# Kernel tuning notes

Hardware: AMD Instinct MI355X
Metric: run time of the kernel (lower is better)

The kernel has to match this reference:

```python
import jax, jax.numpy as jnp
import numpy as np
import math

B, N, IN_DIM = 128, 100, 8
E, H, FF, L = 512, 8, 2048, 6
DH = E // H
MAX_STEPS = int(N * 1.5)
EPS = 1e-5

def _ln(x, g, b):
    mu = x.mean(-1, keepdims=True)
    var = ((x - mu) ** 2).mean(-1, keepdims=True)
    return (x - mu) / jnp.sqrt(var + EPS) * g + b

def _mha(q_in, k_in, v_in, wq, bq, wk, bk, wv, bv, wo, bo):
    Bq, Sq = q_in.shape[0], q_in.shape[1]
    q = (q_in @ wq + bq).reshape(Bq, Sq, H, DH)
    k = (k_in @ wk + bk).reshape(Bq, -1, H, DH)
    v = (v_in @ wv + bv).reshape(Bq, -1, H, DH)
    s = jnp.einsum('bqhd,bkhd->bhqk', q, k) / math.sqrt(DH)
    a = jax.nn.softmax(s, axis=-1)
    o = jnp.einsum('bhqk,bkhd->bqhd', a, v).reshape(Bq, Sq, E)
    return o @ wo + bo

def setup_inputs():
    key = jax.random.key(0)
    keys = iter(jax.random.split(key, 64))
    def nrm(shape, s=0.02):
        return jax.random.normal(next(keys), shape, jnp.float32) * s
    d = {}
    d['node_features'] = jax.random.normal(next(keys), (B, N, IN_DIM), jnp.float32)
    d['edge_weights'] = jax.random.uniform(next(keys), (B, N, N), jnp.float32)
    pos = np.arange(N)[:, None].astype(np.float32)
    div = np.exp(np.arange(0, E, 2).astype(np.float32) * (-math.log(10000.0) / E))
    pe = np.zeros((N, E), np.float32)
    pe[:, 0::2] = np.sin(pos * div); pe[:, 1::2] = np.cos(pos * div)
    d['pe'] = jnp.asarray(pe)
    d['in_w'] = nrm((IN_DIM, E)); d['in_b'] = jnp.zeros((E,), jnp.float32)
    for nm in ['enc_wq', 'enc_wk', 'enc_wv', 'enc_wo']:
        d[nm] = nrm((L, E, E))
    for nm in ['enc_bq', 'enc_bk', 'enc_bv', 'enc_bo']:
        d[nm] = jnp.zeros((L, E), jnp.float32)
    d['enc_w1'] = nrm((L, E, FF)); d['enc_b1'] = jnp.zeros((L, FF), jnp.float32)
    d['enc_w2'] = nrm((L, FF, E)); d['enc_b2'] = jnp.zeros((L, E), jnp.float32)
    d['enc_ln1g'] = jnp.ones((L, E), jnp.float32); d['enc_ln1b'] = jnp.zeros((L, E), jnp.float32)
    d['enc_ln2g'] = jnp.ones((L, E), jnp.float32); d['enc_ln2b'] = jnp.zeros((L, E), jnp.float32)
    d['lstm_wih'] = nrm((E, 4 * E)); d['lstm_whh'] = nrm((E, 4 * E))
    d['lstm_bih'] = jnp.zeros((4 * E,), jnp.float32); d['lstm_bhh'] = jnp.zeros((4 * E,), jnp.float32)
    for nm in ['dec_wq', 'dec_wk', 'dec_wv', 'dec_wo', 'dec_pw']:
        d[nm] = nrm((E, E))
    for nm in ['dec_bq', 'dec_bk', 'dec_bv', 'dec_bo', 'dec_pb']:
        d[nm] = jnp.zeros((E,), jnp.float32)
    d['dec_lng'] = jnp.ones((E,), jnp.float32); d['dec_lnb'] = jnp.zeros((E,), jnp.float32)
    d['shortcut_bonus'] = jnp.asarray(5.0, jnp.float32)
    d['revisit_penalty'] = jnp.asarray(-0.5, jnp.float32)
    d['done_w'] = nrm((E, 1)); d['done_b'] = jnp.zeros((1,), jnp.float32)
    return d

def _forward(node_features, edge_weights, pe, in_w, in_b, enc_wq, enc_bq, enc_wk, enc_bk, enc_wv, enc_bv, enc_wo, enc_bo, enc_w1, enc_b1, enc_w2, enc_b2, enc_ln1g, enc_ln1b, enc_ln2g, enc_ln2b, lstm_wih, lstm_whh, lstm_bih, lstm_bhh, dec_wq, dec_bq, dec_wk, dec_bk, dec_wv, dec_bv, dec_wo, dec_bo, dec_pw, dec_pb, dec_lng, dec_lnb, shortcut_bonus, revisit_penalty, done_w, done_b):
    # ---- Encoder (dropout = eval-mode identity) ----
    x = node_features @ in_w + in_b + pe[:N]
    for l in range(L):
        attn = _mha(x, x, x, enc_wq[l], enc_bq[l], enc_wk[l], enc_bk[l], enc_wv[l], enc_bv[l], enc_wo[l], enc_bo[l])
        x = _ln(x + attn, enc_ln1g[l], enc_ln1b[l])
        ff = jax.nn.relu(x @ enc_w1[l] + enc_b1[l]) @ enc_w2[l] + enc_b2[l]
        x = _ln(x + ff, enc_ln2g[l], enc_ln2b[l])
    node_emb = x  # [B, N, E]

    ar = jnp.arange(N)
    ew_to_first = edge_weights[:, :, 0]  # dist(mid -> node 0), [B, N]

    def step_fn(carry, step):
        h, c, ctx, visited, ucount, complete, all_vis, first, prev = carry
        # LSTMCell, torch gate order (i, f, g, o)
        gates = ctx @ lstm_wih + lstm_bih + h @ lstm_whh + lstm_bhh
        i_g, f_g, g_g, o_g = jnp.split(gates, 4, axis=-1)
        c2 = jax.nn.sigmoid(f_g) * c + jax.nn.sigmoid(i_g) * jnp.tanh(g_g)
        h2 = jax.nn.sigmoid(o_g) * jnp.tanh(c2)
        # greedy done-predictor: stop if sigmoid(logit) > 0.5 once tour can be closed
        done_p = jax.nn.sigmoid(h2 @ done_w + done_b)[:, 0]
        eligible = (~complete) & (ucount >= N) & (step >= N)
        complete = complete | (eligible & (done_p > 0.5))
        # DecoderStep: 1-query attention over node embeddings
        a = _mha(h2[:, None, :], node_emb, node_emb, dec_wq, dec_bq, dec_wk, dec_bk, dec_wv, dec_bv, dec_wo, dec_bo)[:, 0]
        a = _ln(a, dec_lng, dec_lnb)
        logits = a @ dec_pw + dec_pb
        scores = jnp.einsum('be,bne->bn', logits, node_emb)
        # revisit penalty while tour incomplete (vectorized masked_fill_)
        scores = jnp.where((~all_vis)[:, None] & visited, revisit_penalty, scores)
        # shortcut bonus once all nodes visited (vectorized gather over edge_weights)
        ew_prev = jnp.take_along_axis(edge_weights, prev[:, None, None], axis=1)[:, 0, :]  # [B, N] row dist(prev -> *)
        direct = ew_prev[:, :1]                      # dist(prev -> 0)
        via = ew_prev + ew_to_first                  # dist(prev -> mid) + dist(mid -> 0)
        bonus = jnp.where(via < direct, shortcut_bonus * (direct - via) / direct, 0.0)
        scores = scores + jnp.where(all_vis[:, None], bonus, 0.0)
        # completed tours: force return to first node
        scores = jnp.where(complete[:, None], -1e9, scores)
        scores = jnp.where(complete[:, None] & (ar[None, :] == first[:, None]), 100.0, scores)
        probs = jax.nn.softmax(scores, axis=1)
        curr = jnp.argmax(probs, axis=1).astype(jnp.int32)  # greedy selection
        logp = jnp.log(jnp.take_along_axis(probs, curr[:, None], 1)[:, 0] + 1e-10)
        first = jnp.where(step == 0, curr, first)
        # state updates (guarded by active, as in the torch per-batch loop)
        active = ~complete
        cur_mask = ar[None, :] == curr[:, None]
        newly = active & ~jnp.take_along_axis(visited, curr[:, None], 1)[:, 0]
        ucount = ucount + newly.astype(jnp.int32)
        visited = visited | (active[:, None] & cur_mask)
        all_vis = all_vis | (ucount >= N)
        ctx2 = jnp.take_along_axis(node_emb, curr[:, None, None], axis=1)[:, 0, :]
        return (h2, c2, ctx2, visited, ucount, complete, all_vis, first, curr), (curr, logp)

    carry0 = (jnp.zeros((B, E), jnp.float32), jnp.zeros((B, E), jnp.float32), node_emb.mean(1),
              jnp.zeros((B, N), bool), jnp.zeros((B,), jnp.int32),
              jnp.zeros((B,), bool), jnp.zeros((B,), bool),
              jnp.zeros((B,), jnp.int32), jnp.zeros((B,), jnp.int32))
    carry, (tours, logps) = jax.lax.scan(step_fn, carry0, jnp.arange(MAX_STEPS))
    complete, first = carry[5], carry[7]
    # final forced step (step == max_steps in torch): incomplete tours return to first node, logp = 0
    final_node = jnp.where(complete, jnp.int32(0), first)
    tours = jnp.concatenate([tours, final_node[None]], 0)                 # [MAX_STEPS+1, B]
    logps = jnp.concatenate([logps, jnp.zeros((1, B), jnp.float32)], 0)   # [MAX_STEPS+1, B]
    return logps, tours

def reference(node_features, edge_weights, pe, in_w, in_b, enc_wq, enc_bq, enc_wk, enc_bk, enc_wv, enc_bv, enc_wo, enc_bo, enc_w1, enc_b1, enc_w2, enc_b2, enc_ln1g, enc_ln1b, enc_ln2g, enc_ln2b, lstm_wih, lstm_whh, lstm_bih, lstm_bhh, dec_wq, dec_bq, dec_wk, dec_bk, dec_wv, dec_bv, dec_wo, dec_bo, dec_pw, dec_pb, dec_lng, dec_lnb, shortcut_bonus, revisit_penalty, done_w, done_b):
    return _forward(node_features, edge_weights, pe, in_w, in_b, enc_wq, enc_bq, enc_wk, enc_bk, enc_wv, enc_bv, enc_wo, enc_bo, enc_w1, enc_b1, enc_w2, enc_b2, enc_ln1g, enc_ln1b, enc_ln2g, enc_ln2b, lstm_wih, lstm_whh, lstm_bih, lstm_bhh, dec_wq, dec_bq, dec_wk, dec_bk, dec_wv, dec_bv, dec_wo, dec_bo, dec_pw, dec_pb, dec_lng, dec_lnb, shortcut_bonus, revisit_penalty, done_w, done_b)
```

## Files before the change

### kernel.cpp

```cpp
#include <hip/hip_runtime.h>
#include <math.h>

#define Bb 128
#define Nn 100
#define Ee 512
#define Hh 8
#define DHd 64
#define FFf 2048
#define Ll 6
#define STEPS 150

typedef _Float16 h8 __attribute__((ext_vector_type(8)));
typedef _Float16 h4 __attribute__((ext_vector_type(4)));
typedef float f4 __attribute__((ext_vector_type(4)));

template<bool RELU, bool BIAS, bool OUTF32, bool SPLITK>
__global__ __launch_bounds__(256) void mgemm_k(
    const _Float16* __restrict__ Ah, const _Float16* __restrict__ Al, int lda,
    const _Float16* __restrict__ Bh, const _Float16* __restrict__ Bl, int ldb,
    float* __restrict__ C, _Float16* __restrict__ Ch, _Float16* __restrict__ Cl,
    int ldc, const float* __restrict__ bias, int K, int kc, int Mtot)
{
  __shared__ _Float16 sm[4 * 5120];
  _Float16* sAh = sm;
  _Float16* sAl = sm + 5120;
  _Float16* sBh = sm + 10240;
  _Float16* sBl = sm + 15360;
  const int tid = threadIdx.x;
  const int m0 = blockIdx.y * 128, n0 = blockIdx.x * 128;
  const int k0 = SPLITK ? blockIdx.z * kc : 0;
  const int kEnd = SPLITK ? k0 + kc : K;
  const int lane = tid & 63, wave = tid >> 6;
  const int wm = wave >> 1, wn = wave & 1;
  const int m16 = lane & 15, kg = lane >> 4;
  f4 acc[4][4];
#pragma unroll
  for (int i = 0; i < 4; ++i)
#pragma unroll
    for (int j = 0; j < 4; ++j) acc[i][j] = (f4)0.f;

  for (int kt = k0; kt < kEnd; kt += 32) {
#pragma unroll
    for (int it = 0; it < 2; ++it) {
      int idx = tid + it * 256;
      int row = idx >> 2, g = idx & 3;
      int lo_ = row * 40 + g * 8;
      size_t ga = (size_t)(m0 + row) * lda + kt + g * 8;
      size_t gb = (size_t)(n0 + row) * ldb + kt + g * 8;
      *(h8*)(sAh + lo_) = *(const h8*)(Ah + ga);
      *(h8*)(sAl + lo_) = *(const h8*)(Al + ga);
      *(h8*)(sBh + lo_) = *(const h8*)(Bh + gb);
      *(h8*)(sBl + lo_) = *(const h8*)(Bl + gb);
    }
    __syncthreads();
    h8 a_h[4], a_l[4], b_h[4], b_l[4];
#pragma unroll
    for (int i = 0; i < 4; ++i) {
      int ro = (wm * 64 + i * 16 + m16) * 40 + kg * 8;
      int co = (wn * 64 + i * 16 + m16) * 40 + kg * 8;
      a_h[i] = *(const h8*)(sAh + ro);
      a_l[i] = *(const h8*)(sAl + ro);
      b_h[i] = *(const h8*)(sBh + co);
      b_l[i] = *(const h8*)(sBl + co);
    }
#pragma unroll
    for (int i = 0; i < 4; ++i)
#pragma unroll
      for (int j = 0; j < 4; ++j) {
        acc[i][j] = __builtin_amdgcn_mfma_f32_16x16x32_f16(a_h[i], b_h[j], acc[i][j], 0, 0, 0);
        acc[i][j] = __builtin_amdgcn_mfma_f32_16x16x32_f16(a_h[i], b_l[j], acc[i][j], 0, 0, 0);
        acc[i][j] = __builtin_amdgcn_mfma_f32_16x16x32_f16(a_l[i], b_h[j], acc[i][j], 0, 0, 0);
      }
    __syncthreads();
  }

  float* Cz = OUTF32 ? (C + (SPLITK ? (size_t)blockIdx.z * (size_t)Mtot * ldc : (size_t)0)) : C;
  int rb = m0 + wm * 64 + kg * 4;
  int cb = n0 + wn * 64 + m16;
#pragma unroll
  for (int j = 0; j < 4; ++j) {
    int col = cb + j * 16;
    float bv = BIAS ? bias[col] : 0.f;
#pragma unroll
    for (int i = 0; i < 4; ++i) {
#pragma unroll
      for (int r = 0; r < 4; ++r) {
        float v = acc[i][j][r] + bv;
        if (RELU) v = fmaxf(v, 0.f);
        int row = rb + i * 16 + r;
        if (OUTF32) {
          Cz[(size_t)row * ldc + col] = v;
        } else {
          _Float16 hh = (_Float16)v;
          Ch[(size_t)row * ldc + col] = hh;
          Cl[(size_t)row * ldc + col] = (_Float16)(v - (float)hh);
        }
      }
    }
  }
}

__global__ __launch_bounds__(256) void wconv_k(
    const float* __restrict__ W, int K, int N,
    _Float16* __restrict__ Th, _Float16* __restrict__ Tl)
{
  __shared__ float t[32][33];
  int n0 = blockIdx.x * 32, k0 = blockIdx.y * 32;
  int tid = threadIdx.x;
  int r = tid >> 3, c4 = (tid & 7) * 4;
  float4 v = *(const float4*)(W + (size_t)(k0 + r) * N + n0 + c4);
  t[r][c4 + 0] = v.x; t[r][c4 + 1] = v.y; t[r][c4 + 2] = v.z; t[r][c4 + 3] = v.w;
  __syncthreads();
  h4 hi, lo;
#pragma unroll
// ... 76 lines not shown
  const float* qg = q + ((size_t)b * Nn) * 512 + h * 64;
  const float* kg = k + ((size_t)b * Nn) * 512 + h * 64;
  const float* vg = v + ((size_t)b * Nn) * 512 + h * 64;
  for (int idx = t; idx < 6400; idx += 256) {
    int i = idx >> 6, d = idx & 63;
    qs[i * 68 + d]  = qg[(size_t)i * 512 + d];
    kT[d * 113 + i] = kg[(size_t)i * 512 + d];
  }
  __syncthreads();
  int ti = t >> 4, tj = t & 15;
  int i0 = ti * 7, j0 = tj * 7;
  float s[7][7];
#pragma unroll
  for (int r = 0; r < 7; ++r)
#pragma unroll
    for (int c = 0; c < 7; ++c) s[r][c] = 0.f;
  for (int kk = 0; kk < 64; ++kk) {
    float a[7], bb[7];
#pragma unroll
    for (int r = 0; r < 7; ++r) a[r] = qs[(i0 + r) * 68 + kk];
#pragma unroll
    for (int c = 0; c < 7; ++c) bb[c] = kT[kk * 113 + j0 + c];
#pragma unroll
    for (int r = 0; r < 7; ++r)
#pragma unroll
      for (int c = 0; c < 7; ++c) s[r][c] += a[r] * bb[c];
  }
  __syncthreads();
#pragma unroll
  for (int r = 0; r < 7; ++r)
#pragma unroll
    for (int c = 0; c < 7; ++c) {
      int i = i0 + r, j = j0 + c;
      if (i < Nn && j < Nn) p[i * 104 + j] = s[r][c] * 0.125f;
    }
  __syncthreads();
  int w = t >> 6, lane = t & 63;
  for (int i = w; i < Nn; i += 4) {
    float x0 = p[i * 104 + lane];
    float x1 = (lane < 36) ? p[i * 104 + 64 + lane] : -3.4e38f;
    float mx = fmaxf(x0, x1);
    for (int msk = 32; msk; msk >>= 1) mx = fmaxf(mx, __shfl_xor(mx, msk));
    float e0 = expf(x0 - mx);
    float e1 = (lane < 36) ? expf(x1 - mx) : 0.f;
    float ss = e0 + e1;
    for (int msk = 32; msk; msk >>= 1) ss += __shfl_xor(ss, msk);
    p[i * 104 + lane] = e0 / ss;
    if (lane < 36) p[i * 104 + 64 + lane] = e1 / ss;
  }
  __syncthreads();
  int d0 = tj * 4;
  float oa[7][4];
#pragma unroll
  for (int r = 0; r < 7; ++r)
#pragma unroll
    for (int c = 0; c < 4; ++c) oa[r][c] = 0.f;
  for (int j = 0; j < Nn; ++j) {
    float pr[7];
#pragma unroll
    for (int r = 0; r < 7; ++r) pr[r] = p[(i0 + r) * 104 + j];
    float4 vv = *(const float4*)(vg + (size_t)j * 512 + d0);
#pragma unroll
    for (int r = 0; r < 7; ++r) {
      oa[r][0] += pr[r] * vv.x; oa[r][1] += pr[r] * vv.y;
      oa[r][2] += pr[r] * vv.z; oa[r][3] += pr[r] * vv.w;
    }
  }
  size_t ob = ((size_t)b * Nn) * 512 + h * 64 + d0;
#pragma unroll
  for (int r = 0; r < 7; ++r)
    if (i0 + r < Nn) {
      h4 hv, lv;
#pragma unroll
      for (int c = 0; c < 4; ++c) {
        _Float16 hh = (_Float16)oa[r][c];
        hv[c] = hh;
        lv[c] = (_Float16)(oa[r][c] - (float)hh);
      }
      *(h4*)(oh + ob + (size_t)(i0 + r) * 512) = hv;
      *(h4*)(ol + ob + (size_t)(i0 + r) * 512) = lv;
    }
}

template<int BM, int BN, int BK, int TM, int TN>
__global__ __launch_bounds__(256) void gemm_k(
    const float* __restrict__ A, int lda,
    const float* __restrict__ B1, const float* __restrict__ B2, int splitB, int ldb,
    float* __restrict__ C, int ldc, int M, int N, int K, int kChunk)
{
  __shared__ __align__(16) float As[BK][BM + 4];
  __shared__ __align__(16) float Bs[BK][BN + 4];
  const int tid = threadIdx.x;
  const int m0 = blockIdx.y * BM;
  const int n0 = blockIdx.x * BN;
  const int k0 = blockIdx.z * kChunk;
  const int kEnd = k0 + kChunk;
  constexpr int TCOLS = BN / TN;
  const int tm = tid / TCOLS;
  const int tn = tid % TCOLS;
  float acc[TM][TN];
#pragma unroll
  for (int i = 0; i < TM; ++i)
#pragma unroll
    for (int j = 0; j < TN; ++j) acc[i][j] = 0.f;

  for (int kt = k0; kt < kEnd; kt += BK) {
    constexpr int A4 = BM * BK / 4;
    for (int c = tid; c < A4; c += 256) {
      int mm = c / (BK / 4);
      int k4 = (c % (BK / 4)) * 4;
      float4 av = *(const float4*)(A + (size_t)(m0 + mm) * lda + kt + k4);
      As[k4 + 0][mm] = av.x;
      As[k4 + 1][mm] = av.y;
      As[k4 + 2][mm] = av.z;
      As[k4 + 3][mm] = av.w;
    }
    constexpr int B4 = BK * BN / 4;
    for (int c = tid; c < B4; c += 256) {
      int kk = c / (BN / 4);
      int n4 = (c % (BN / 4)) * 4;
      int kgi = kt + kk;
      const float* Brow = (kgi < splitB) ? (B1 + (size_t)kgi * ldb)
                                         : (B2 + (size_t)(kgi - splitB) * ldb);
      *(float4*)&Bs[kk][n4] = *(const float4*)(Brow + n0 + n4);
    }
    __syncthreads();
#pragma unroll
    for (int kk = 0; kk < BK; ++kk) {
      float a[TM], b[TN];
#pragma unroll
      for (int i = 0; i < TM; ++i) a[i] = As[kk][tm * TM + i];
#pragma unroll
      for (int j = 0; j < TN; ++j) b[j] = Bs[kk][tn * TN + j];
#pragma unroll
      for (int i = 0; i < TM; ++i)
#pragma unroll
        for (int j = 0; j < TN; ++j)
          acc[i][j] += a[i] * b[j];
    }
    __syncthreads();
  }

  float* Cout = C + (size_t)blockIdx.z * (size_t)M * ldc;
#pragma unroll
  for (int i = 0; i < TM; ++i) {
    int m = m0 + tm * TM + i;
#pragma unroll
    for (int j = 0; j < TN; j += 4) {
      int n = n0 + tn * TN + j;
      float4 r;
      r.x = acc[i][j + 0]; r.y = acc[i][j + 1]; r.z = acc[i][j + 2]; r.w = acc[i][j + 3];
      *(float4*)(Cout + (size_t)m * ldc + n) = r;
    }
  }
}

__global__ __launch_bounds__(256) void init_k(
    const float* __restrict__ emb, float* __restrict__ ctxh, float* __restrict__ cbuf,
    int* visited, int* ucount, int* complete, int* allvis, int* first, int* prev,
    float* out)
{
  int b = blockIdx.x, t = threadIdx.x;
#pragma unroll
  for (int r = 0; r < 2; ++r) {
    int e = t + 256 * r;
    float s = 0.f;
    for (int i = 0; i < Nn; ++i) s += emb[((size_t)b * Nn + i) * 512 + e];
    ctxh[(size_t)b * 1024 + e] = s / 100.f;
    ctxh[(size_t)b * 1024 + 512 + e] = 0.f;
    cbuf[(size_t)b * 512 + e] = 0.f;
  }
  if (t < Nn) visited[b * Nn + t] = 0;
  if (t == 0) {
    ucount[b] = 0; complete[b] = 0; allvis[b] = 0; first[b] = 0; prev[b] = 0;
    out[150 * Bb + b] = 0.f;
  }
}

__device__ __forceinline__ float sigm(float x) { return 1.f / (1.f + expf(-x)); }

__global__ __launch_bounds__(256) void lstm_pw_k(
    const float* __restrict__ gP, const float* __restrict__ bih, const float* __restrict__ bhh,
    float* __restrict__ ctxh, float* __restrict__ cbuf,
    const float* __restrict__ done_w, const float* __restrict__ done_b,
    int* complete, const int* ucount, int step)
{
  int b = blockIdx.x, t = threadIdx.x;
  __shared__ float red[256];
  const float* g0 = gP + (size_t)b * 2048;
  const float* g1 = gP + 262144 + (size_t)b * 2048;
  float dsum = 0.f;
#pragma unroll
  for (int r = 0; r < 2; ++r) {
    int e = t + 256 * r;
    float ig = g0[e] + g1[e] + bih[e] + bhh[e];
    float fg = g0[e + 512] + g1[e + 512] + bih[e + 512] + bhh[e + 512];
    float gg = g0[e + 1024] + g1[e + 1024] + bih[e + 1024] + bhh[e + 1024];
    float og = g0[e + 1536] + g1[e + 1536] + bih[e + 1536] + bhh[e + 1536];
    float cprev = cbuf[(size_t)b * 512 + e];
    float c2 = sigm(fg) * cprev + sigm(ig) * tanhf(gg);
    float h2 = sigm(og) * tanhf(c2);
    cbuf[(size_t)b * 512 + e] = c2;
    ctxh[(size_t)b * 1024 + 512 + e] = h2;
    dsum += h2 * done_w[e];
  }
  red[t] = dsum; __syncthreads();
  for (int o = 128; o > 0; o >>= 1) { if (t < o) red[t] += red[t + o]; __syncthreads(); }
  if (t == 0) {
    float z = red[0] + done_b[0];
    if (!complete[b] && ucount[b] >= Nn && step >= Nn && z > 0.f) complete[b] = 1;
  }
}

__global__ __launch_bounds__(128) void dec_attn_k(
    const float* __restrict__ qP, const float* __restrict__ bq,
    const float* __restrict__ Kd, const float* __restrict__ Vd,
    float* __restrict__ o)
{
  int bh = blockIdx.x; int b = bh >> 3, h = bh & 7;
  int t = threadIdx.x;
  __shared__ float qh[64];
  __shared__ float p[100];
  __shared__ float red[128];
  if (t < 64) {
    float s = bq[h * 64 + t];
#pragma unroll
    for (int s8 = 0; s8 < 8; ++s8) s += qP[(size_t)s8 * 65536 + (size_t)b * 512 + h * 64 + t];
    qh[t] = s;
  }
  __syncthreads();
  float scv = -3.4e38f;
  if (t < Nn) {
    const float* kr = Kd + ((size_t)b * Nn + t) * 512 + h * 64;
    float s = 0.f;
#pragma unroll
    for (int d = 0; d < 64; ++d) s += qh[d] * kr[d];
    scv = s * 0.125f;
  }
  red[t] = scv; __syncthreads();
  for (int o2 = 64; o2 > 0; o2 >>= 1) { if (t < o2) red[t] = fmaxf(red[t], red[t + o2]); __syncthreads(); }
  float m = red[0]; __syncthreads();
  float ex = (t < Nn) ? expf(scv - m) : 0.f;
  red[t] = ex; __syncthreads();
  for (int o2 = 64; o2 > 0; o2 >>= 1) { if (t < o2) red[t] += red[t + o2]; __syncthreads(); }
  float Z = red[0];
  if (t < Nn) p[t] = ex / Z;
  __syncthreads();
  if (t < 64) {
    float acc = 0.f;
    const float* vr = Vd + (size_t)b * Nn * 512 + h * 64 + t;
    for (int j = 0; j < Nn; ++j) acc += p[j] * vr[(size_t)j * 512];
    o[(size_t)b * 512 + h * 64 + t] = acc;
  }
}

__global__ __launch_bounds__(256) void dec_ln_k(
    const float* __restrict__ woP, const float* __restrict__ bo,
    const float* __restrict__ g, const float* __restrict__ bb,
    float* __restrict__ out)
{
  int b = blockIdx.x, t = threadIdx.x;
  __shared__ float red[256];
  float v[2];
#pragma unroll
  for (int r = 0; r < 2; ++r) {
    int e = t + 256 * r;
    float s = bo[e];
#pragma unroll
    for (int s8 = 0; s8 < 8; ++s8) s += woP[(size_t)s8 * 65536 + (size_t)b * 512 + e];
    v[r] = s;
  }
  red[t] = v[0] + v[1]; __syncthreads();
  for (int o = 128; o > 0; o >>= 1) { if (t < o) red[t] += red[t + o]; __syncthreads(); }
  float mu = red[0] * (1.f / 512.f);
  __syncthreads();
  float d0 = v[0] - mu, d1 = v[1] - mu;
  red[t] = d0 * d0 + d1 * d1; __syncthreads();
  for (int o = 128; o > 0; o >>= 1) { if (t < o) red[t] += red[t + o]; __syncthreads(); }
  float inv = 1.f / sqrtf(red[0] * (1.f / 512.f) + 1e-5f);
  out[(size_t)b * 512 + t] = d0 * inv * g[t] + bb[t];
  out[(size_t)b * 512 + t + 256] = d1 * inv * g[t + 256] + bb[t + 256];
}

__global__ __launch_bounds__(256) void select_k(
    const float* __restrict__ pwP, const float* __restrict__ pb,
    const float* __restrict__ emb, const float* __restrict__ ew,
    int* visited, int* ucount, int* complete, int* allvis, int* first, int* prev,
    float* __restrict__ ctxh, float* __restrict__ out,
    const float* __restrict__ sb_p, const float* __restrict__ rp_p, int step)
{
  int b = blockIdx.x, t = threadIdx.x;
  __shared__ float logits[512];
  __shared__ float sc[128];
  __shared__ float red[256];
  __shared__ int redi[256];
#pragma unroll
  for (int r = 0; r < 2; ++r) {
    int e = t + 256 * r;
    float s = pb[e];
#pragma unroll
    for (int s8 = 0; s8 < 8; ++s8) s += pwP[(size_t)s8 * 65536 + (size_t)b * 512 + e];
    logits[e] = s;
  }
  __syncthreads();
  if (t < Nn) {
    const float* er = emb + ((size_t)b * Nn + t) * 512;
    float s = 0.f;
    for (int e = 0; e < 512; ++e) s += logits[e] * er[e];
    int av = allvis[b];
    if (!av && visited[b * Nn + t]) s = rp_p[0];
    if (av) {
      int pv = prev[b];
      float direct = ew[(size_t)b * 10000 + (size_t)pv * 100];
      float via = ew[(size_t)b * 10000 + (size_t)pv * 100 + t] + ew[(size_t)b * 10000 + (size_t)t * 100];
      if (via < direct) s += sb_p[0] * (direct - via) / direct;
    }
    if (complete[b]) s = (t == first[b]) ? 100.f : -1e9f;
    sc[t] = s;
  }
  __syncthreads();
  float vv = (t < Nn) ? sc[t] : -3.4e38f;
  int ii = (t < Nn) ? t : 0x7fffffff;
  red[t] = vv; redi[t] = ii;
  __syncthreads();
  for (int o = 128; o > 0; o >>= 1) {
    if (t < o) {
      float v2 = red[t + o]; int i2 = redi[t + o];
      if (v2 > red[t] || (v2 == red[t] && i2 < redi[t])) { red[t] = v2; redi[t] = i2; }
    }
    __syncthreads();
  }
  float m = red[0];
  int curr = redi[0];
  __syncthreads();
  float ex = (t < Nn) ? expf(sc[t] - m) : 0.f;
  red[t] = ex; __syncthreads();
  for (int o = 128; o > 0; o >>= 1) { if (t < o) red[t] += red[t + o]; __syncthreads(); }
  float Z = red[0];
  if (t == 0) {
    float pcur = expf(sc[curr] - m) / Z;
    out[step * Bb + b] = logf(pcur + 1e-10f);
    out[(151 + step) * Bb + b] = (float)curr;
    if (!complete[b]) {
      if (!visited[b * Nn + curr]) ucount[b] = ucount[b] + 1;
      visited[b * Nn + curr] = 1;
    }
    if (ucount[b] >= Nn) allvis[b] = 1;
    if (step == 0) first[b] = curr;
    prev[b] = curr;
  }
  const float* src = emb + ((size_t)b * Nn + curr) * 512;
  ctxh[(size_t)b * 1024 + t] = src[t];
  ctxh[(size_t)b * 1024 + t + 256] = src[t + 256];
}

__global__ void final_k(const int* complete, const int* first, float* out)
{
  int b = threadIdx.x;
  out[(151 + 150) * Bb + b] = complete[b] ? 0.f : (float)first[b];
}

extern "C" void kernel_launch(void* const* d_in, const int* in_sizes, int n_in,
                              void* d_out, int out_size, void* d_ws, size_t ws_size,
                              hipStream_t stream)
{
  const float* nf      = (const float*)d_in[0];
  const float* ew      = (const float*)d_in[1];
  const float* pe      = (const float*)d_in[2];
  const float* in_w    = (const float*)d_in[3];
  const float* in_b    = (const float*)d_in[4];
  const float* enc_wq  = (const float*)d_in[5];
  const float* enc_wk  = (const float*)d_in[6];
  const float* enc_wv  = (const float*)d_in[7];
  const float* enc_wo  = (const float*)d_in[8];
  const float* enc_bq  = (const float*)d_in[9];
  const float* enc_bk  = (const float*)d_in[10];
  const float* enc_bv  = (const float*)d_in[11];
  const float* enc_bo  = (const float*)d_in[12];
  const float* enc_w1  = (const float*)d_in[13];
  const float* enc_b1  = (const float*)d_in[14];
  const float* enc_w2  = (const float*)d_in[15];
  const float* enc_b2  = (const float*)d_in[16];
  const float* ln1g    = (const float*)d_in[17];
  const float* ln1b    = (const float*)d_in[18];
  const float* ln2g    = (const float*)d_in[19];
  const float* ln2b    = (const float*)d_in[20];
  const float* wih     = (const float*)d_in[21];
  const float* whh     = (const float*)d_in[22];
  const float* bih     = (const float*)d_in[23];
  const float* bhh     = (const float*)d_in[24];
  const float* dwq     = (const float*)d_in[25];
  const float* dwk     = (const float*)d_in[26];
  const float* dwv     = (const float*)d_in[27];
  const float* dwo     = (const float*)d_in[28];
  const float* dpw     = (const float*)d_in[29];
  const float* dbq     = (const float*)d_in[30];
  const float* dbk     = (const float*)d_in[31];
  const float* dbv     = (const float*)d_in[32];
  const float* dbo     = (const float*)d_in[33];
  const float* dpb     = (const float*)d_in[34];
  const float* dlng    = (const float*)d_in[35];
  const float* dlnb    = (const float*)d_in[36];
  const float* sbp     = (const float*)d_in[37];
  const float* rpp     = (const float*)d_in[38];
  const float* done_w  = (const float*)d_in[39];
  const float* done_b  = (const float*)d_in[40];
  float* out = (float*)d_out;

  const size_t SZ = 12800ull * 512;
  float* ws = (float*)d_ws;
  float* x   = ws;
  float* xq  = x + SZ;
  float* xk  = xq + SZ;
  float* xv  = xk + SZ;
  _Float16* xh = (_Float16*)(xv + SZ);
  _Float16* xl = xh + SZ;
  _Float16* oh = xl + SZ;
  _Float16* ol = oh + SZ;
  _Float16* wb = ol + SZ;
  _Float16* wqh = wb;               _Float16* wql = wqh + 262144;
  _Float16* wkh = wql + 262144;     _Float16* wkl = wkh + 262144;
  _Float16* wvh = wkl + 262144;     _Float16* wvl = wvh + 262144;
  _Float16* woh_ = wvl + 262144;    _Float16* wol_ = woh_ + 262144;
  _Float16* w1h = wol_ + 262144;    _Float16* w1l = w1h + 1048576;
  _Float16* w2h = w1l + 1048576;    _Float16* w2l = w2h + 1048576;
  float* ctxh   = (float*)(w2l + 1048576);
  float* cbuf   = ctxh + 131072;
  float* gatesP = cbuf + 65536;
  float* qP     = gatesP + 524288;
  float* woP    = qP + 524288;
  float* pwP    = woP + 524288;
  float* abuf   = pwP + 524288;
  float* dbuf   = abuf + 65536;
  int* ivis     = (int*)(dbuf + 65536);
  int* ucount   = ivis + 12800;
  int* complete = ucount + 128;
  int* allvis   = complete + 128;
  int* first    = allvis + 128;
  int* prev     = first + 128;

  input_proj_k<<<25600, 256, 0, stream>>>(nf, in_w, in_b, pe, x, xh, xl);

  for (int l = 0; l < Ll; ++l) {
    const float* wq = enc_wq + (size_t)l * 262144;
    const float* wk = enc_wk + (size_t)l * 262144;
    const float* wv = enc_wv + (size_t)l * 262144;
    const float* wo = enc_wo + (size_t)l * 262144;
    const float* bq = enc_bq + (size_t)l * 512;
    const float* bk = enc_bk + (size_t)l * 512;
    const float* bv = enc_bv + (size_t)l * 512;
    const float* bo = enc_bo + (size_t)l * 512;
    const float* w1 = enc_w1 + (size_t)l * 1048576;
    const float* b1 = enc_b1 + (size_t)l * 2048;
    const float* w2 = enc_w2 + (size_t)l * 1048576;
    const float* b2 = enc_b2 + (size_t)l * 512;

    wconv_k<<<dim3(16, 16), 256, 0, stream>>>(wq, 512, 512, wqh, wql);
    wconv_k<<<dim3(16, 16), 256, 0, stream>>>(wk, 512, 512, wkh, wkl);
    wconv_k<<<dim3(16, 16), 256, 0, stream>>>(wv, 512, 512, wvh, wvl);
    wconv_k<<<dim3(16, 16), 256, 0, stream>>>(wo, 512, 512, woh_, wol_);
    wconv_k<<<dim3(64, 16), 256, 0, stream>>>(w1, 512, 2048, w1h, w1l);
    wconv_k<<<dim3(16, 64), 256, 0, stream>>>(w2, 2048, 512, w2h, w2l);

    mgemm_k<false, true, true, false><<<dim3(4, 100), 256, 0, stream>>>(
        xh, xl, 512, wqh, wql, 512, xq, nullptr, nullptr, 512, bq, 512, 0, 0);
    mgemm_k<false, true, true, false><<<dim3(4, 100), 256, 0, stream>>>(
        xh, xl, 512, wkh, wkl, 512, xk, nullptr, nullptr, 512, bk, 512, 0, 0);
    mgemm_k<false, true, true, false><<<dim3(4, 100), 256, 0, stream>>>(
        xh, xl, 512, wvh, wvl, 512, xv, nullptr, nullptr, 512, bv, 512, 0, 0);
    enc_attn_k<<<1024, 256, 0, stream>>>(xq, xk, xv, oh, ol);
    mgemm_k<false, true, true, false><<<dim3(4, 100), 256, 0, stream>>>(
        oh, ol, 512, woh_, wol_, 512, xq, nullptr, nullptr, 512, bo, 512, 0, 0);
    ln_k<<<12800, 256, 0, stream>>>(x, xq, ln1g + l * 512, ln1b + l * 512, x, xh, xl);
    for (int c = 0; c < 4; ++c) {
      mgemm_k<true, true, false, false><<<dim3(16, 25), 256, 0, stream>>>(
          xh + (size_t)c * 3200 * 512, xl + (size_t)c * 3200 * 512, 512,
          w1h, w1l, 512, nullptr, oh, ol, 2048, b1, 512, 0, 0);
      mgemm_k<false, false, true, true><<<dim3(4, 25, 4), 256, 0, stream>>>(
          oh, ol, 2048, w2h, w2l, 2048, xv, nullptr, nullptr, 512,
          nullptr, 2048, 512, 3200);
      reduce4_k<<<6400, 256, 0, stream>>>(xv, b2, xq + (size_t)c * 3200 * 512);
    }
    ln_k<<<12800, 256, 0, stream>>>(x, xq, ln2g + l * 512, ln2b + l * 512, x, xh, xl);
  }

  wconv_k<<<dim3(16, 16), 256, 0, stream>>>(dwk, 512, 512, wqh, wql);
  wconv_k<<<dim3(16, 16), 256, 0, stream>>>(dwv, 512, 512, wkh, wkl);
  mgemm_k<false, true, true, false><<<dim3(4, 100), 256, 0, stream>>>(
      xh, xl, 512, wqh, wql, 512, xk, nullptr, nullptr, 512, dbk, 512, 0, 0);
  mgemm_k<false, true, true, false><<<dim3(4, 100), 256, 0, stream>>>(
      xh, xl, 512, wkh, wkl, 512, xv, nullptr, nullptr, 512, dbv, 512, 0, 0);
  init_k<<<128, 256, 0, stream>>>(x, ctxh, cbuf, ivis, ucount, complete, allvis, first, prev, out);

  for (int step = 0; step < STEPS; ++step) {
    gemm_k<32, 64, 16, 2, 4><<<dim3(32, 4, 2), 256, 0, stream>>>(
        ctxh, 1024, wih, whh, 512, 2048, gatesP, 2048, 128, 2048, 1024, 512);
    lstm_pw_k<<<128, 256, 0, stream>>>(gatesP, bih, bhh, ctxh, cbuf, done_w, done_b,
                                       complete, ucount, step);
    gemm_k<32, 64, 16, 2, 4><<<dim3(8, 4, 8), 256, 0, stream>>>(
        ctxh + 512, 1024, dwq, dwq, 1 << 30, 512, qP, 512, 128, 512, 512, 64);
    dec_attn_k<<<1024, 128, 0, stream>>>(qP, dbq, xk, xv, dbuf);
    gemm_k<32, 64, 16, 2, 4><<<dim3(8, 4, 8), 256, 0, stream>>>(
        dbuf, 512, dwo, dwo, 1 << 30, 512, woP, 512, 128, 512, 512, 64);
    dec_ln_k<<<128, 256, 0, stream>>>(woP, dbo, dlng, dlnb, abuf);
    gemm_k<32, 64, 16, 2, 4><<<dim3(8, 4, 8), 256, 0, stream>>>(
        abuf, 512, dpw, dpw, 1 << 30, 512, pwP, 512, 128, 512, 512, 64);
    select_k<<<128, 256, 0, stream>>>(pwP, dpb, x, ew, ivis, ucount, complete, allvis,
                                      first, prev, ctxh, out, sbp, rpp, step);
  }
  final_k<<<1, 128, 0, stream>>>(complete, first, out);
}
```

Baseline: 16.51 ms.

## Fuse decode loop into a persistent kernel with global atomic barriers

Replaces the per-step sequence of eight small decoder kernel launches with a single persistent kernel of 128 blocks that loops over all steps. Each former kernel becomes a phase separated by a device-wide barrier built from agent-scope atomics, and each block handles two GEMM tiles per phase. This targets launch and inter-kernel gap overhead on the serial decode loop. In exchange, parallelism per phase drops, every phase pays a spin-barrier cost, and correctness depends on all blocks being co-resident.

```diff
diff --git a/kernel.cpp b/kernel.cpp
--- a/kernel.cpp
+++ b/kernel.cpp
@@ -9,6 +9,7 @@
 #define FFf 2048
 #define Ll 6
 #define STEPS 150
+#define NBLK 128
 
 typedef _Float16 h8 __attribute__((ext_vector_type(8)));
 typedef _Float16 h4 __attribute__((ext_vector_type(4)));
@@ -29,7 +30,7 @@
   const int tid = threadIdx.x;
   const int m0 = blockIdx.y * 128, n0 = blockIdx.x * 128;
   const int k0 = SPLITK ? blockIdx.z * kc : 0;
-  const int kEnd = SPLITK ? k0 + kc : K;
+  const int kEnd = SPLITK ? (k0 + kc) : K;
   const int lane = tid & 63, wave = tid >> 6;
   const int wm = wave >> 1, wn = wave & 1;
   const int m16 = lane & 15, kg = lane >> 4;
@@ -272,83 +273,10 @@
     }
 }
 
-template<int BM, int BN, int BK, int TM, int TN>
-__global__ __launch_bounds__(256) void gemm_k(
-    const float* __restrict__ A, int lda,
-    const float* __restrict__ B1, const float* __restrict__ B2, int splitB, int ldb,
-    float* __restrict__ C, int ldc, int M, int N, int K, int kChunk)
-{
-  __shared__ __align__(16) float As[BK][BM + 4];
-  __shared__ __align__(16) float Bs[BK][BN + 4];
-  const int tid = threadIdx.x;
-  const int m0 = blockIdx.y * BM;
-  const int n0 = blockIdx.x * BN;
-  const int k0 = blockIdx.z * kChunk;
-  const int kEnd = k0 + kChunk;
-  constexpr int TCOLS = BN / TN;
-  const int tm = tid / TCOLS;
-  const int tn = tid % TCOLS;
-  float acc[TM][TN];
-#pragma unroll
-  for (int i = 0; i < TM; ++i)
-#pragma unroll
-    for (int j = 0; j < TN; ++j) acc[i][j] = 0.f;
-
-  for (int kt = k0; kt < kEnd; kt += BK) {
-    constexpr int A4 = BM * BK / 4;
-    for (int c = tid; c < A4; c += 256) {
-      int mm = c / (BK / 4);
-      int k4 = (c % (BK / 4)) * 4;
-      float4 av = *(const float4*)(A + (size_t)(m0 + mm) * lda + kt + k4);
-      As[k4 + 0][mm] = av.x;
-      As[k4 + 1][mm] = av.y;
-      As[k4 + 2][mm] = av.z;
-      As[k4 + 3][mm] = av.w;
-    }
-    constexpr int B4 = BK * BN / 4;
-    for (int c = tid; c < B4; c += 256) {
-      int kk = c / (BN / 4);
-      int n4 = (c % (BN / 4)) * 4;
-      int kgi = kt + kk;
-      const float* Brow = (kgi < splitB) ? (B1 + (size_t)kgi * ldb)
-                                         : (B2 + (size_t)(kgi - splitB) * ldb);
-      *(float4*)&Bs[kk][n4] = *(const float4*)(Brow + n0 + n4);
-    }
-    __syncthreads();
-#pragma unroll
-    for (int kk = 0; kk < BK; ++kk) {
-      float a[TM], b[TN];
-#pragma unroll
-      for (int i = 0; i < TM; ++i) a[i] = As[kk][tm * TM + i];
-#pragma unroll
-      for (int j = 0; j < TN; ++j) b[j] = Bs[kk][tn * TN + j];
-#pragma unroll
-      for (int i = 0; i < TM; ++i)
-#pragma unroll
-        for (int j = 0; j < TN; ++j)
-          acc[i][j] += a[i] * b[j];
-    }
-    __syncthreads();
-  }
-
-  float* Cout = C + (size_t)blockIdx.z * (size_t)M * ldc;
-#pragma unroll
-  for (int i = 0; i < TM; ++i) {
-    int m = m0 + tm * TM + i;
-#pragma unroll
-    for (int j = 0; j < TN; j += 4) {
-      int n = n0 + tn * TN + j;
-      float4 r;
-      r.x = acc[i][j + 0]; r.y = acc[i][j + 1]; r.z = acc[i][j + 2]; r.w = acc[i][j + 3];
-      *(float4*)(Cout + (size_t)m * ldc + n) = r;
-    }
-  }
-}
-
 __global__ __launch_bounds__(256) void init_k(
     const float* __restrict__ emb, float* __restrict__ ctxh, float* __restrict__ cbuf,
     int* visited, int* ucount, int* complete, int* allvis, int* first, int* prev,
-    float* out)
+    int* bars, float* out)
 {
   int b = blockIdx.x, t = threadIdx.x;
 #pragma unroll
@@ -365,189 +293,312 @@
     ucount[b] = 0; complete[b] = 0; allvis[b] = 0; first[b] = 0; prev[b] = 0;
     out[150 * Bb + b] = 0.f;
   }
+  for (int i = b * 256 + t; i < 1280; i += 128 * 256) bars[i] = 0;
 }
 
 __device__ __forceinline__ float sigm(float x) { return 1.f / (1.f + expf(-x)); }
 
-__global__ __launch_bounds__(256) void lstm_pw_k(
-    const float* __restrict__ gP, const float* __restrict__ bih, const float* __restrict__ bhh,
-    float* __restrict__ ctxh, float* __restrict__ cbuf,
-    const float* __restrict__ done_w, const float* __restrict__ done_b,
-    int* complete, const int* ucount, int step)
-{
-  int b = blockIdx.x, t = threadIdx.x;
-  __shared__ float red[256];
-  const float* g0 = gP + (size_t)b * 2048;
-  const float* g1 = gP + 262144 + (size_t)b * 2048;
-  float dsum = 0.f;
-#pragma unroll
-  for (int r = 0; r < 2; ++r) {
-    int e = t + 256 * r;
-    float ig = g0[e] + g1[e] + bih[e] + bhh[e];
-    float fg = g0[e + 512] + g1[e + 512] + bih[e + 512] + bhh[e + 512];
-    float gg = g0[e + 1024] + g1[e + 1024] + bih[e + 1024] + bhh[e + 1024];
-    float og = g0[e + 1536] + g1[e + 1536] + bih[e + 1536] + bhh[e + 1536];
-    float cprev = cbuf[(size_t)b * 512 + e];
-    float c2 = sigm(fg) * cprev + sigm(ig) * tanhf(gg);
-    float h2 = sigm(og) * tanhf(c2);
-    cbuf[(size_t)b * 512 + e] = c2;
-    ctxh[(size_t)b * 1024 + 512 + e] = h2;
-    dsum += h2 * done_w[e];
-  }
-  red[t] = dsum; __syncthreads();
-  for (int o = 128; o > 0; o >>= 1) { if (t < o) red[t] += red[t + o]; __syncthreads(); }
-  if (t == 0) {
-    float z = red[0] + done_b[0];
-    if (!complete[b] && ucount[b] >= Nn && step >= Nn && z > 0.f) complete[b] = 1;
-  }
-}
-
-__global__ __launch_bounds__(128) void dec_attn_k(
-    const float* __restrict__ qP, const float* __restrict__ bq,
-    const float* __restrict__ Kd, const float* __restrict__ Vd,
-    float* __restrict__ o)
-{
-  int bh = blockIdx.x; int b = bh >> 3, h = bh & 7;
-  int t = threadIdx.x;
-  __shared__ float qh[64];
-  __shared__ float p[100];
-  __shared__ float red[128];
-  if (t < 64) {
-    float s = bq[h * 64 + t];
-#pragma unroll
-    for (int s8 = 0; s8 < 8; ++s8) s += qP[(size_t)s8 * 65536 + (size_t)b * 512 + h * 64 + t];
-    qh[t] = s;
-  }
-  __syncthreads();
-  float scv = -3.4e38f;
-  if (t < Nn) {
-    const float* kr = Kd + ((size_t)b * Nn + t) * 512 + h * 64;
-    float s = 0.f;
-#pragma unroll
-    for (int d = 0; d < 64; ++d) s += qh[d] * kr[d];
-    scv = s * 0.125f;
-  }
-  red[t] = scv; __syncthreads();
-  for (int o2 = 64; o2 > 0; o2 >>= 1) { if (t < o2) red[t] = fmaxf(red[t], red[t + o2]); __syncthreads(); }
-  float m = red[0]; __syncthreads();
-  float ex = (t < Nn) ? expf(scv - m) : 0.f;
-  red[t] = ex; __syncthreads();
-  for (int o2 = 64; o2 > 0; o2 >>= 1) { if (t < o2) red[t] += red[t + o2]; __syncthreads(); }
-  float Z = red[0];
-  if (t < Nn) p[t] = ex / Z;
-  __syncthreads();
-  if (t < 64) {
-    float acc = 0.f;
-    const float* vr = Vd + (size_t)b * Nn * 512 + h * 64 + t;
-    for (int j = 0; j < Nn; ++j) acc += p[j] * vr[(size_t)j * 512];
-    o[(size_t)b * 512 + h * 64 + t] = acc;
-  }
-}
-
-__global__ __launch_bounds__(256) void dec_ln_k(
-    const float* __restrict__ woP, const float* __restrict__ bo,
-    const float* __restrict__ g, const float* __restrict__ bb,
-    float* __restrict__ out)
-{
-  int b = blockIdx.x, t = threadIdx.x;
-  __shared__ float red[256];
-  float v[2];
-#pragma unroll
-  for (int r = 0; r < 2; ++r) {
-    int e = t + 256 * r;
-    float s = bo[e];
-#pragma unroll
-    for (int s8 = 0; s8 < 8; ++s8) s += woP[(size_t)s8 * 65536 + (size_t)b * 512 + e];
-    v[r] = s;
-  }
-  red[t] = v[0] + v[1]; __syncthreads();
-  for (int o = 128; o > 0; o >>= 1) { if (t < o) red[t] += red[t + o]; __syncthreads(); }
-  float mu = red[0] * (1.f / 512.f);
-  __syncthreads();
-  float d0 = v[0] - mu, d1 = v[1] - mu;
-  red[t] = d0 * d0 + d1 * d1; __syncthreads();
-  for (int o = 128; o > 0; o >>= 1) { if (t < o) red[t] += red[t + o]; __syncthreads(); }
-  float inv = 1.f / sqrtf(red[0] * (1.f / 512.f) + 1e-5f);
-  out[(size_t)b * 512 + t] = d0 * inv * g[t] + bb[t];
-  out[(size_t)b * 512 + t + 256] = d1 * inv * g[t + 256] + bb[t + 256];
-}
-
-__global__ __launch_bounds__(256) void select_k(
-    const float* __restrict__ pwP, const float* __restrict__ pb,
-    const float* __restrict__ emb, const float* __restrict__ ew,
-    int* visited, int* ucount, int* complete, int* allvis, int* first, int* prev,
-    float* __restrict__ ctxh, float* __restrict__ out,
-    const float* __restrict__ sb_p, const float* __restrict__ rp_p, int step)
-{
-  int b = blockIdx.x, t = threadIdx.x;
-  __shared__ float logits[512];
-  __shared__ float sc[128];
-  __shared__ float red[256];
-  __shared__ int redi[256];
-#pragma unroll
-  for (int r = 0; r < 2; ++r) {
-    int e = t + 256 * r;
-    float s = pb[e];
-#pragma unroll
-    for (int s8 = 0; s8 < 8; ++s8) s += pwP[(size_t)s8 * 65536 + (size_t)b * 512 + e];
-    logits[e] = s;
-  }
-  __syncthreads();
-  if (t < Nn) {
-    const float* er = emb + ((size_t)b * Nn + t) * 512;
-    float s = 0.f;
-    for (int e = 0; e < 512; ++e) s += logits[e] * er[e];
-    int av = allvis[b];
-    if (!av && visited[b * Nn + t]) s = rp_p[0];
-    if (av) {
-      int pv = prev[b];
-      float direct = ew[(size_t)b * 10000 + (size_t)pv * 100];
-      float via = ew[(size_t)b * 10000 + (size_t)pv * 100 + t] + ew[(size_t)b * 10000 + (size_t)t * 100];
-      if (via < direct) s += sb_p[0] * (direct - via) / direct;
-    }
-    if (complete[b]) s = (t == first[b]) ? 100.f : -1e9f;
-    sc[t] = s;
-  }
-  __syncthreads();
-  float vv = (t < Nn) ? sc[t] : -3.4e38f;
-  int ii = (t < Nn) ? t : 0x7fffffff;
-  red[t] = vv; redi[t] = ii;
-  __syncthreads();
-  for (int o = 128; o > 0; o >>= 1) {
-    if (t < o) {
-      float v2 = red[t + o]; int i2 = redi[t + o];
-      if (v2 > red[t] || (v2 == red[t] && i2 < redi[t])) { red[t] = v2; redi[t] = i2; }
+__device__ __forceinline__ void gbar(int* bars, int slot)
+{
+  __syncthreads();
+  if (threadIdx.x == 0) {
+    __threadfence();
+    __hip_atomic_fetch_add(&bars[slot], 1, __ATOMIC_RELEASE, __HIP_MEMORY_SCOPE_AGENT);
+    while (__hip_atomic_load(&bars[slot], __ATOMIC_ACQUIRE, __HIP_MEMORY_SCOPE_AGENT) < NBLK)
+      __builtin_amdgcn_s_sleep(1);
+    __threadfence();
+  }
+  __syncthreads();
+}
+
+__device__ void gemm_dev(
+    int bx, int by, int bz,
+    const float* __restrict__ A, int lda,
+    const float* __restrict__ B1, const float* __restrict__ B2, int splitB, int ldb,
+    float* __restrict__ C, int ldc, int kChunk, char* smraw)
+{
+  float (*As)[36] = (float(*)[36])smraw;
+  float (*Bs)[68] = (float(*)[68])(smraw + 2304);
+  const int tid = threadIdx.x;
+  const int m0 = by * 32, n0 = bx * 64;
+  const int k0 = bz * kChunk, kEnd = k0 + kChunk;
+  const int tm = tid >> 4, tn = tid & 15;
+  float acc[2][4];
+#pragma unroll
+  for (int i = 0; i < 2; ++i)
+#pragma unroll
+    for (int j = 0; j < 4; ++j) acc[i][j] = 0.f;
+
+  for (int kt = k0; kt < kEnd; kt += 16) {
+    for (int c = tid; c < 128; c += 256) {
+      int mm = c >> 2;
+      int k4 = (c & 3) * 4;
+      float4 av = *(const float4*)(A + (size_t)(m0 + mm) * lda + kt + k4);
+      As[k4 + 0][mm] = av.x;
+      As[k4 + 1][mm] = av.y;
+      As[k4 + 2][mm] = av.z;
+      As[k4 + 3][mm] = av.w;
+    }
+    for (int c = tid; c < 256; c += 256) {
+      int kk = c >> 4;
+      int n4 = (c & 15) * 4;
+      int kgi = kt + kk;
+      const float* Brow = (kgi < splitB) ? (B1 + (size_t)kgi * ldb)
+                                         : (B2 + (size_t)(kgi - splitB) * ldb);
+      *(float4*)&Bs[kk][n4] = *(const float4*)(Brow + n0 + n4);
     }
     __syncthreads();
-  }
-  float m = red[0];
-  int curr = redi[0];
-  __syncthreads();
-  float ex = (t < Nn) ? expf(sc[t] - m) : 0.f;
-  red[t] = ex; __syncthreads();
-  for (int o = 128; o > 0; o >>= 1) { if (t < o) red[t] += red[t + o]; __syncthreads(); }
-  float Z = red[0];
-  if (t == 0) {
-    float pcur = expf(sc[curr] - m) / Z;
-    out[step * Bb + b] = logf(pcur + 1e-10f);
-    out[(151 + step) * Bb + b] = (float)curr;
-    if (!complete[b]) {
-      if (!visited[b * Nn + curr]) ucount[b] = ucount[b] + 1;
-      visited[b * Nn + curr] = 1;
-    }
-    if (ucount[b] >= Nn) allvis[b] = 1;
-    if (step == 0) first[b] = curr;
-    prev[b] = curr;
-  }
-  const float* src = emb + ((size_t)b * Nn + curr) * 512;
-  ctxh[(size_t)b * 1024 + t] = src[t];
-  ctxh[(size_t)b * 1024 + t + 256] = src[t + 256];
-}
-
-__global__ void final_k(const int* complete, const int* first, float* out)
-{
-  int b = threadIdx.x;
-  out[(151 + 150) * Bb + b] = complete[b] ? 0.f : (float)first[b];
+#pragma unroll
+    for (int kk = 0; kk < 16; ++kk) {
+      float a[2], b[4];
+#pragma unroll
+      for (int i = 0; i < 2; ++i) a[i] = As[kk][tm * 2 + i];
+#pragma unroll
+      for (int j = 0; j < 4; ++j) b[j] = Bs[kk][tn * 4 + j];
+#pragma unroll
+      for (int i = 0; i < 2; ++i)
+#pragma unroll
+        for (int j = 0; j < 4; ++j)
+          acc[i][j] += a[i] * b[j];
+    }
+    __syncthreads();
+  }
+
+  float* Cout = C + (size_t)bz * 128 * ldc;
+#pragma unroll
+  for (int i = 0; i < 2; ++i) {
+    int m = m0 + tm * 2 + i;
+    int n = n0 + tn * 4;
+    float4 r;
+    r.x = acc[i][0]; r.y = acc[i][1]; r.z = acc[i][2]; r.w = acc[i][3];
+    *(float4*)(Cout + (size_t)m * ldc + n) = r;
+  }
+}
+
+struct DP {
+  float *ctxh, *cbuf, *gatesP, *qP, *woP, *pwP, *abuf, *dbuf;
+  const float *emb, *Kd, *Vd, *ew;
+  const float *wih, *whh, *bih, *bhh;
+  const float *dwq, *dbq, *dwo, *dbo, *dlng, *dlnb, *dpw, *dpb;
+  const float *done_w, *done_b, *sbp, *rpp;
+  int *visited, *ucount, *complete, *allvis, *first, *prev, *bars;
+  float *out;
+};
+
+__global__ __launch_bounds__(256, 1) void decode_pers_k(DP P)
+{
+  const int bid = blockIdx.x;
+  const int t = threadIdx.x;
+  __shared__ __align__(16) char smraw[6912];
+  const int BIG = 1 << 30;
+  int slot = 0;
+
+  for (int step = 0; step < STEPS; ++step) {
+#pragma unroll 1
+    for (int v = 0; v < 2; ++v) {
+      int vb = bid * 2 + v;
+      gemm_dev(vb & 31, (vb >> 5) & 3, vb >> 7,
+               P.ctxh, 1024, P.wih, P.whh, 512, 2048,
+               P.gatesP, 2048, 512, smraw);
+    }
+    gbar(P.bars, slot++);
+
+    {
+      int b = bid;
+      float* red = (float*)smraw;
+      const float* g0 = P.gatesP + (size_t)b * 2048;
+      const float* g1 = P.gatesP + 262144 + (size_t)b * 2048;
+      float dsum = 0.f;
+#pragma unroll
+      for (int r = 0; r < 2; ++r) {
+        int e = t + 256 * r;
+        float ig = g0[e] + g1[e] + P.bih[e] + P.bhh[e];
+        float fg = g0[e + 512] + g1[e + 512] + P.bih[e + 512] + P.bhh[e + 512];
+        float gg = g0[e + 1024] + g1[e + 1024] + P.bih[e + 1024] + P.bhh[e + 1024];
+        float og = g0[e + 1536] + g1[e + 1536] + P.bih[e + 1536] + P.bhh[e + 1536];
+        float cprev = P.cbuf[(size_t)b * 512 + e];
+        float c2 = sigm(fg) * cprev + sigm(ig) * tanhf(gg);
+        float h2 = sigm(og) * tanhf(c2);
+        P.cbuf[(size_t)b * 512 + e] = c2;
+        P.ctxh[(size_t)b * 1024 + 512 + e] = h2;
+        dsum += h2 * P.done_w[e];
+      }
+      red[t] = dsum; __syncthreads();
+      for (int o = 128; o > 0; o >>= 1) { if (t < o) red[t] += red[t + o]; __syncthreads(); }
+      if (t == 0) {
+        float z = red[0] + P.done_b[0];
+        if (!P.complete[b] && P.ucount[b] >= Nn && step >= Nn && z > 0.f) P.complete[b] = 1;
+      }
+    }
+    gbar(P.bars, slot++);
+
+#pragma unroll 1
+    for (int v = 0; v < 2; ++v) {
+      int vb = bid * 2 + v;
+      gemm_dev(vb & 7, (vb >> 3) & 3, vb >> 5,
+               P.ctxh + 512, 1024, P.dwq, P.dwq, BIG, 512,
+               P.qP, 512, 64, smraw);
+    }
+    gbar(P.bars, slot++);
+
+    {
+      int half = t >> 7, tl = t & 127;
+      float* qh = (float*)smraw + half * 320;
+      float* pv = qh + 64;
+      float* red = pv + 128;
+#pragma unroll 1
+      for (int r4 = 0; r4 < 4; ++r4) {
+        int item = bid * 8 + r4 * 2 + half;
+        int b = item >> 3, h = item & 7;
+        if (tl < 64) {
+          float s = P.dbq[h * 64 + tl];
+#pragma unroll
+          for (int z = 0; z < 8; ++z) s += P.qP[(size_t)z * 65536 + (size_t)b * 512 + h * 64 + tl];
+          qh[tl] = s;
+        }
+        __syncthreads();
+        float scv = -3.4e38f;
+        if (tl < Nn) {
+          const float* kr = P.Kd + ((size_t)(b * Nn + tl)) * 512 + h * 64;
+          float s = 0.f;
+#pragma unroll
+          for (int d = 0; d < 64; ++d) s += qh[d] * kr[d];
+          scv = s * 0.125f;
+        }
+        red[tl] = scv; __syncthreads();
+        for (int o2 = 64; o2 > 0; o2 >>= 1) { if (tl < o2) red[tl] = fmaxf(red[tl], red[tl + o2]); __syncthreads(); }
+        float m = red[0]; __syncthreads();
+        float ex = (tl < Nn) ? expf(scv - m) : 0.f;
+        red[tl] = ex; __syncthreads();
+        for (int o2 = 64; o2 > 0; o2 >>= 1) { if (tl < o2) red[tl] += red[tl + o2]; __syncthreads(); }
+        float Z = red[0];
+        if (tl < Nn) pv[tl] = ex / Z;
+        __syncthreads();
+        if (tl < 64) {
+          float acc = 0.f;
+          const float* vr = P.Vd + (size_t)(b * Nn) * 512 + h * 64 + tl;
+          for (int j = 0; j < Nn; ++j) acc += pv[j] * vr[(size_t)j * 512];
+          P.dbuf[(size_t)b * 512 + h * 64 + tl] = acc;
+        }
+        __syncthreads();
+      }
+    }
+    gbar(P.bars, slot++);
+
+#pragma unroll 1
+    for (int v = 0; v < 2; ++v) {
+      int vb = bid * 2 + v;
+      gemm_dev(vb & 7, (vb >> 3) & 3, vb >> 5,
+               P.dbuf, 512, P.dwo, P.dwo, BIG, 512,
+               P.woP, 512, 64, smraw);
+    }
+    gbar(P.bars, slot++);
+
+    {
+      int b = bid;
+      float* red = (float*)smraw;
+      float v[2];
+#pragma unroll
+      for (int r = 0; r < 2; ++r) {
+        int e = t + 256 * r;
+        float s = P.dbo[e];
+#pragma unroll
+        for (int s8 = 0; s8 < 8; ++s8) s += P.woP[(size_t)s8 * 65536 + (size_t)b * 512 + e];
+        v[r] = s;
+      }
+      red[t] = v[0] + v[1]; __syncthreads();
+      for (int o = 128; o > 0; o >>= 1) { if (t < o) red[t] += red[t + o]; __syncthreads(); }
+      float mu = red[0] * (1.f / 512.f);
+      __syncthreads();
+      float d0 = v[0] - mu, d1 = v[1] - mu;
+      red[t] = d0 * d0 + d1 * d1; __syncthreads();
+      for (int o = 128; o > 0; o >>= 1) { if (t < o) red[t] += red[t + o]; __syncthreads(); }
+      float inv = 1.f / sqrtf(red[0] * (1.f / 512.f) + 1e-5f);
+      P.abuf[(size_t)b * 512 + t] = d0 * inv * P.dlng[t] + P.dlnb[t];
+      P.abuf[(size_t)b * 512 + t + 256] = d1 * inv * P.dlng[t + 256] + P.dlnb[t + 256];
+    }
+    gbar(P.bars, slot++);
+
+#pragma unroll 1
+    for (int v = 0; v < 2; ++v) {
+      int vb = bid * 2 + v;
+      gemm_dev(vb & 7, (vb >> 3) & 3, vb >> 5,
+               P.abuf, 512, P.dpw, P.dpw, BIG, 512,
+               P.pwP, 512, 64, smraw);
+    }
+    gbar(P.bars, slot++);
+
+    {
+      int b = bid;
+      float* logits = (float*)smraw;
+      float* sc = logits + 512;
+      float* red = sc + 128;
+      int* redi = (int*)(red + 256);
+#pragma unroll
+      for (int r = 0; r < 2; ++r) {
+        int e = t + 256 * r;
+        float s = P.dpb[e];
+#pragma unroll
+        for (int s8 = 0; s8 < 8; ++s8) s += P.pwP[(size_t)s8 * 65536 + (size_t)b * 512 + e];
+        logits[e] = s;
+      }
+      __syncthreads();
+      if (t < Nn) {
+        const float* er = P.emb + ((size_t)(b * Nn + t)) * 512;
+        float s = 0.f;
+        for (int e = 0; e < 512; ++e) s += logits[e] * er[e];
+        int av = P.allvis[b];
+        if (!av && P.visited[b * Nn + t]) s = P.rpp[0];
+        if (av) {
+          int pv = P.prev[b];
+          float direct = P.ew[(size_t)b * 10000 + (size_t)pv * 100];
+          float via = P.ew[(size_t)b * 10000 + (size_t)pv * 100 + t]
+                    + P.ew[(size_t)b * 10000 + (size_t)t * 100];
+          if (via < direct) s += P.sbp[0] * (direct - via) / direct;
+        }
+        if (P.complete[b]) s = (t == P.first[b]) ? 100.f : -1e9f;
+        sc[t] = s;
+      }
+      __syncthreads();
+      float vv = (t < Nn) ? sc[t] : -3.4e38f;
+      int ii = (t < Nn) ? t : 0x7fffffff;
+      red[t] = vv; redi[t] = ii;
+      __syncthreads();
+      for (int o = 128; o > 0; o >>= 1) {
+        if (t < o) {
+          float v2 = red[t + o]; int i2 = redi[t + o];
+          if (v2 > red[t] || (v2 == red[t] && i2 < redi[t])) { red[t] = v2; redi[t] = i2; }
+        }
+        __syncthreads();
+      }
+      float m = red[0];
+      int curr = redi[0];
+      __syncthreads();
+      float ex = (t < Nn) ? expf(sc[t] - m) : 0.f;
+      red[t] = ex; __syncthreads();
+      for (int o = 128; o > 0; o >>= 1) { if (t < o) red[t] += red[t + o]; __syncthreads(); }
+      float Z = red[0];
+      if (t == 0) {
+        float pcur = expf(sc[curr] - m) / Z;
+        P.out[step * Bb + b] = logf(pcur + 1e-10f);
+        P.out[(151 + step) * Bb + b] = (float)curr;
+        if (!P.complete[b]) {
+          if (!P.visited[b * Nn + curr]) P.ucount[b] = P.ucount[b] + 1;
+          P.visited[b * Nn + curr] = 1;
+        }
+        if (P.ucount[b] >= Nn) P.allvis[b] = 1;
+        if (step == 0) P.first[b] = curr;
+        P.prev[b] = curr;
+      }
+      const float* src = P.emb + ((size_t)(b * Nn) + (size_t)curr) * 512;
+      P.ctxh[(size_t)b * 1024 + t] = src[t];
+      P.ctxh[(size_t)b * 1024 + t + 256] = src[t + 256];
+    }
+    gbar(P.bars, slot++);
+  }
+
+  if (bid == 0 && t < 128)
+    P.out[(151 + 150) * Bb + t] = P.complete[t] ? 0.f : (float)P.first[t];
 }
 
 extern "C" void kernel_launch(void* const* d_in, const int* in_sizes, int n_in,
@@ -628,6 +679,7 @@
   int* allvis   = complete + 128;
   int* first    = allvis + 128;
   int* prev     = first + 128;
+  int* bars     = prev + 128;
 
   input_proj_k<<<25600, 256, 0, stream>>>(nf, in_w, in_b, pe, x, xh, xl);
 
@@ -680,23 +732,19 @@
       xh, xl, 512, wqh, wql, 512, xk, nullptr, nullptr, 512, dbk, 512, 0, 0);
   mgemm_k<false, true, true, false><<<dim3(4, 100), 256, 0, stream>>>(
       xh, xl, 512, wkh, wkl, 512, xv, nullptr, nullptr, 512, dbv, 512, 0, 0);
-  init_k<<<128, 256, 0, stream>>>(x, ctxh, cbuf, ivis, ucount, complete, allvis, first, prev, out);
-
-  for (int step = 0; step < STEPS; ++step) {
-    gemm_k<32, 64, 16, 2, 4><<<dim3(32, 4, 2), 256, 0, stream>>>(
-        ctxh, 1024, wih, whh, 512, 2048, gatesP, 2048, 128, 2048, 1024, 512);
-    lstm_pw_k<<<128, 256, 0, stream>>>(gatesP, bih, bhh, ctxh, cbuf, done_w, done_b,
-                                       complete, ucount, step);
-    gemm_k<32, 64, 16, 2, 4><<<dim3(8, 4, 8), 256, 0, stream>>>(
-        ctxh + 512, 1024, dwq, dwq, 1 << 30, 512, qP, 512, 128, 512, 512, 64);
-    dec_attn_k<<<1024, 128, 0, stream>>>(qP, dbq, xk, xv, dbuf);
-    gemm_k<32, 64, 16, 2, 4><<<dim3(8, 4, 8), 256, 0, stream>>>(
-        dbuf, 512, dwo, dwo, 1 << 30, 512, woP, 512, 128, 512, 512, 64);
-    dec_ln_k<<<128, 256, 0, stream>>>(woP, dbo, dlng, dlnb, abuf);
-    gemm_k<32, 64, 16, 2, 4><<<dim3(8, 4, 8), 256, 0, stream>>>(
-        abuf, 512, dpw, dpw, 1 << 30, 512, pwP, 512, 128, 512, 512, 64);
-    select_k<<<128, 256, 0, stream>>>(pwP, dpb, x, ew, ivis, ucount, complete, allvis,
-                                      first, prev, ctxh, out, sbp, rpp, step);
-  }
-  final_k<<<1, 128, 0, stream>>>(complete, first, out);
-}
+  init_k<<<128, 256, 0, stream>>>(x, ctxh, cbuf, ivis, ucount, complete, allvis,
+                                  first, prev, bars, out);
+
+  DP p;
+  p.ctxh = ctxh; p.cbuf = cbuf; p.gatesP = gatesP; p.qP = qP;
+  p.woP = woP; p.pwP = pwP; p.abuf = abuf; p.dbuf = dbuf;
+  p.emb = x; p.Kd = xk; p.Vd = xv; p.ew = ew;
+  p.wih = wih; p.whh = whh; p.bih = bih; p.bhh = bhh;
+  p.dwq = dwq; p.dbq = dbq; p.dwo = dwo; p.dbo = dbo;
+  p.dlng = dlng; p.dlnb = dlnb; p.dpw = dpw; p.dpb = dpb;
+  p.done_w = done_w; p.done_b = done_b; p.sbp = sbp; p.rpp = rpp;
+  p.visited = ivis; p.ucount = ucount; p.complete = complete;
+  p.allvis = allvis; p.first = first; p.prev = prev; p.bars = bars;
+  p.out = out;
+  decode_pers_k<<<NBLK, 256, 0, stream>>>(p);
+}
```

Measured after the change: 36.09 ms. 2.19x slower.
